# Performance work log

Measured on AMD Instinct MI355X. Metric: run time of the kernel, lower is better.

## Reference

```python
import jax, jax.numpy as jnp
import numpy as np

B, T, D = 32, 512, 240
HF, PF = 1024, 512
HB, PB = 1024, 512
BWD_BLOCK = 32
CLIP = 1.0


def setup_inputs() -> dict:
    key = jax.random.key(0)
    ks = jax.random.split(key, 8)
    u = lambda k, shape: jax.random.uniform(k, shape, jnp.float32, -0.05, 0.05)
    return {
        "data": jax.random.normal(ks[0], (B, T, D), jnp.float32),
        "mask": jnp.ones((B, T), jnp.float32),
        "weight_x_fwd": u(ks[1], (4 * HF, D)),
        "weight_r_fwd": u(ks[2], (4 * HF, PF)),
        "weight_bias_fwd": jnp.zeros((1, 4 * HF), jnp.float32),
        "weight_p_fwd": u(ks[3], (PF, HF)),
        "weight_x_bwd": u(ks[4], (4 * HB, D)),
        "weight_r_bwd": u(ks[5], (4 * HB, PB)),
        "weight_bias_bwd": jnp.zeros((1, 4 * HB), jnp.float32),
        "weight_p_bwd": u(ks[6], (PB, HB)),
    }


def _lstmp_scan(xg, wr, wp, mask, clip, hidden):
    """LSTM-with-projection scan.
    xg:   [T, N, 4H] precomputed input-side gate pre-activations (incl. bias)
    wr:   [4H, P] recurrent weights acting on projected state
    wp:   [P, H] projection weights
    mask: [T, N, 1] float mask (state held where mask==0)
    """
    N = xg.shape[1]
    P = wp.shape[0]
    c0 = jnp.zeros((N, hidden), xg.dtype)
    r0 = jnp.zeros((N, P), xg.dtype)

    def step(carry, inp):
        c, r = carry
        gx, m = inp
        gates = gx + r @ wr.T                      # [N, 4H]
        i, f, g, o = jnp.split(gates, 4, axis=-1)
        i = jax.nn.sigmoid(i)
        f = jax.nn.sigmoid(f)
        g = jnp.tanh(g)
        o = jax.nn.sigmoid(o)
        c_new = jnp.clip(f * c + i * g, -clip, clip)  # cell clipping
        r_new = (o * jnp.tanh(c_new)) @ wp.T          # project H -> P
        c = m * c_new + (1.0 - m) * c
        r = m * r_new + (1.0 - m) * r
        return (c, r), r

    _, rs = jax.lax.scan(step, (c0, r0), (xg, mask))
    return rs  # [T, N, P]


def reference(data, mask, weight_x_fwd, weight_r_fwd, weight_bias_fwd, weight_p_fwd,
              weight_x_bwd, weight_r_bwd, weight_bias_bwd, weight_p_bwd):
    Bx, Tx, _ = data.shape
    m = mask[..., None]  # [B, T, 1]

    # ---- forward direction: full left-to-right scan ----
    xg_f = jnp.einsum('btd,gd->tbg', data, weight_x_fwd) + weight_bias_fwd[0]
    m_f = jnp.swapaxes(m, 0, 1)  # [T, B, 1]
    out_f = _lstmp_scan(xg_f, weight_r_fwd, weight_p_fwd, m_f, CLIP, HF)
    out_f = jnp.swapaxes(out_f, 0, 1)  # [B, T, PF]

    # ---- backward direction: right-to-left within blocks of BWD_BLOCK ----
    L = BWD_BLOCK
    nb = Tx // L
    xg_b = jnp.einsum('btd,gd->btg', data, weight_x_bwd) + weight_bias_bwd[0]
    # split into blocks and reverse time within each block; blocks become batch
    xg_b = xg_b.reshape(Bx, nb, L, 4 * HB)[:, :, ::-1]
    xg_b = xg_b.transpose(2, 0, 1, 3).reshape(L, Bx * nb, 4 * HB)
    m_b = m.reshape(Bx, nb, L, 1)[:, :, ::-1].transpose(2, 0, 1, 3).reshape(L, Bx * nb, 1)
    out_b = _lstmp_scan(xg_b, weight_r_bwd, weight_p_bwd, m_b, CLIP, HB)
    out_b = out_b.reshape(L, Bx, nb, PB).transpose(1, 2, 0, 3)[:, :, ::-1]
    out_b = out_b.reshape(Bx, Tx, PB)

    return jnp.concatenate([out_f, out_b], axis=-1)  # [B, T, PF+PB]
```

## Files before the change

kernel.cpp:

```cpp
#include <hip/hip_runtime.h>
#include <hip/hip_bf16.h>
#include <math.h>


typedef __bf16 bf16_t;
typedef __bf16 bf16x8 __attribute__((ext_vector_type(8)));
typedef float f32x4 __attribute__((ext_vector_type(4)));
typedef unsigned int uint32;
typedef unsigned long long u64;

#define DEV __device__ __forceinline__

DEV bf16x8 ldg8(const bf16_t* p) { return *reinterpret_cast<const bf16x8*>(p); }
DEV bf16x8 ld_llc8(const bf16_t* p) {
  union { bf16x8 v; u64 q[2]; } u;
  u64* pp = (u64*)p;
  u.q[0] = __hip_atomic_load(pp, __ATOMIC_RELAXED, __HIP_MEMORY_SCOPE_AGENT);
  u.q[1] = __hip_atomic_load(pp + 1, __ATOMIC_RELAXED, __HIP_MEMORY_SCOPE_AGENT);
  return u.v;
}
DEV void st_llc_u32(uint32* p, uint32 v) {
  __hip_atomic_store(p, v, __ATOMIC_RELAXED, __HIP_MEMORY_SCOPE_AGENT);
}
DEV f32x4 mfma16(bf16x8 a, bf16x8 b, f32x4 c) {
  return __builtin_amdgcn_mfma_f32_16x16x32_bf16(a, b, c, 0, 0, 0);
}
DEV float sigmoidf_(float x) { return 1.0f / (1.0f + __expf(-x)); }
DEV unsigned short bfbits(float x) {
  union { __bf16 b; unsigned short s; } u; u.b = (bf16_t)x; return u.s;
}

struct Params {
  const float* data;
  const float* mask;
  const float* wx_f; const float* wr_f; const float* bias_f; const float* wp_f;
  const float* wx_b; const float* wr_b; const float* bias_b; const float* wp_b;
  float* out;
  bf16_t* data_bf;
  bf16_t* Wf;
  bf16_t* Wb;
  bf16_t* wrf;
  bf16_t* wpT;
  bf16_t* wpf;
  bf16_t* wpb;
  float* bias_f_p;
  float* bias_b_p;
  bf16_t* h_hist;
  bf16_t* h_buf;
  bf16_t* r_buf;
  f32x4*  chb;
  int* fcnt;
  int* bcA;
  int* bcC;
};

DEV void poll_ge(int* p, int tgt) {
  while (__hip_atomic_load(p, __ATOMIC_RELAXED, __HIP_MEMORY_SCOPE_AGENT) < tgt)
    __builtin_amdgcn_s_sleep(1);
}
DEV void wait_slots(int* base, int nslots, int tgt, int tid) {
  if (tid < nslots) poll_ge(base + tid * 32, tgt);
  __syncthreads();
  asm volatile("" ::: "memory");
}
DEV void drain_sync() {
  asm volatile("s_waitcnt vmcnt(0)" ::: "memory");
  __syncthreads();
}
DEV void pub_add(int* slot) {
  __hip_atomic_fetch_add(slot, 1, __ATOMIC_RELAXED, __HIP_MEMORY_SCOPE_AGENT);
}

__global__ void k_data(Params P) {
  int idx = blockIdx.x * 256 + threadIdx.x;
  int k = idx & 255; int row = idx >> 8;
  float v = (k < 240) ? P.data[(size_t)row * 240 + k] : 0.0f;
  P.data_bf[idx] = (bf16_t)v;
}

__global__ void k_prep_w(Params P) {
  int idx = blockIdx.x * 256 + threadIdx.x;
  int n = 4096 * 512;
  if (idx < n) { P.wrf[idx] = (bf16_t)P.wr_f[idx]; return; }
  idx -= n; n = 1024 * 512;
  if (idx < n) { int h = idx >> 9, p = idx & 511;
                 P.wpT[idx] = (bf16_t)P.wp_f[(size_t)p * 1024 + h]; return; }
  idx -= n; n = 512 * 1024;
  if (idx < n) { P.wpf[idx] = (bf16_t)P.wp_f[idx]; return; }
  idx -= n; n = 512 * 1024;
  if (idx < n) { P.wpb[idx] = (bf16_t)P.wp_b[idx]; return; }
}

__global__ void k_packf(Params P) {
  int pr = blockIdx.x, k = threadIdx.x;
  int jj = pr >> 5, lr = pr & 31, grp = lr >> 3, uu = lr & 7;
  int grow = grp * 1024 + jj * 8 + uu;
  float v = (k < 240) ? P.wx_f[(size_t)grow * 240 + k] : 0.0f;
  P.Wf[(size_t)pr * 1280 + 1024 + k] = (bf16_t)v;
  if (k == 0) P.bias_f_p[pr] = P.bias_f[grow];
}

__global__ void k_packb(Params P) {
  int pr = blockIdx.x; int k = blockIdx.y * 256 + threadIdx.x;
  int ut = pr >> 8, rem = pr & 255, grp = rem >> 6, uu = rem & 63;
  int grow = grp * 1024 + ut * 64 + uu;
  float v;
  if (k < 512) v = P.wr_b[(size_t)grow * 512 + k];
  else { int kx = k - 512; v = (kx < 240) ? P.wx_b[(size_t)grow * 240 + kx] : 0.0f; }
  P.Wb[(size_t)pr * 768 + k] = (bf16_t)v;
  if (k == 0) P.bias_b_p[pr] = P.bias_b[grow];
}

__global__ void wc_gemm(Params P) {
  int tid = threadIdx.x, lane = tid & 63, wave = tid >> 6;
  int lane15 = lane & 15, laneh = lane >> 4;
  int mt = blockIdx.x >> 4, nt = blockIdx.x & 15;
  f32x4 acc[4] = {};
  for (int kc = 0; kc < 16; ++kc) {
    int kl = kc * 32 + laneh * 8;
    bf16x8 bv = ldg8(P.wpT + (size_t)(nt * 64 + wave * 16 + lane15) * 512 + kl);
#pragma unroll
    for (int mh = 0; mh < 4; ++mh) {
      bf16x8 av = ldg8(P.wrf + (size_t)(mt * 64 + mh * 16 + lane15) * 512 + kl);
      acc[mh] = mfma16(av, bv, acc[mh]);
    }
  }
#pragma unroll
  for (int mh = 0; mh < 4; ++mh)
#pragma unroll
    for (int q = 0; q < 4; ++q) {
      int m = mt * 64 + mh * 16 + laneh * 4 + q;
      int grp = m >> 10, unit = m & 1023, jj = unit >> 3, u8 = unit & 7;
      int pr = jj * 32 + grp * 8 + u8;
      int ncol = nt * 64 + wave * 16 + lane15;
      P.Wf[(size_t)pr * 1280 + ncol] = (bf16_t)acc[mh][q];
    }
}

__global__ void __launch_bounds__(256, 1) scan_kernel(Params P) {
  __shared__ union SM {
    float red[4][2][2][16][16];
    float gates[4][64][64];
  } sm;
  const int tid = threadIdx.x;
  const int lane = tid & 63, wave = tid >> 6;
  const int lane15 = lane & 15, laneh = lane >> 4;

  if (blockIdx.x < 128) {
    const int j = blockIdx.x;
    const bf16_t* Wfp = P.Wf + (size_t)(j * 32) * 1280;
    bf16x8 wh[2][8], wx[2][2];
#pragma unroll
    for (int nh = 0; nh < 2; ++nh) {
#pragma unroll
      for (int kc = 0; kc < 8; ++kc)
        wh[nh][kc] = ldg8(Wfp + (size_t)(nh * 16 + lane15) * 1280 +
                          wave * 256 + kc * 32 + laneh * 8);
#pragma unroll
      for (int kc = 0; kc < 2; ++kc)
        wx[nh][kc] = ldg8(Wfp + (size_t)(nh * 16 + lane15) * 1280 +
                          1024 + wave * 64 + kc * 32 + laneh * 8);
    }
    const int cb = tid >> 2, up = tid & 3;
    float biasr[2][4];
    if (tid < 128) {
#pragma unroll
      for (int e = 0; e < 2; ++e)
#pragma unroll
        for (int g = 0; g < 4; ++g)
          biasr[e][g] = P.bias_f_p[j * 32 + g * 8 + 2 * up + e];
    }
    float c_st[2] = {0.f, 0.f}, h_st[2] = {0.f, 0.f};

    for (int t = 0; t < 512; ++t) {
      f32x4 acc[2][2] = {};
      {
        bf16x8 ax[2][2];
#pragma unroll
        for (int kc = 0; kc < 2; ++kc) {
          int kx = wave * 64 + kc * 32 + laneh * 8;
          ax[0][kc] = ldg8(P.data_bf + ((size_t)(lane15 * 512 + t)) * 256 + kx);
          ax[1][kc] = ldg8(P.data_bf + ((size_t)((16 + lane15) * 512 + t)) * 256 + kx);
        }
#pragma unroll
        for (int kc = 0; kc < 2; ++kc)
#pragma unroll
          for (int m = 0; m < 2; ++m) {
            acc[m][0] = mfma16(ax[m][kc], wx[0][kc], acc[m][0]);
            acc[m][1] = mfma16(ax[m][kc], wx[1][kc], acc[m][1]);
          }
      }
      if (t > 0) {
        wait_slots(P.fcnt + (size_t)(t - 1) * 512, 16, 8, tid);
        const bf16_t* hrow = P.h_hist + (size_t)(t - 1) * 32768;
        bf16x8 ah[2][8];
#pragma unroll
        for (int kc = 0; kc < 8; ++kc) {
          int kl = wave * 256 + kc * 32 + laneh * 8;
          ah[0][kc] = ldg8(hrow + (size_t)lane15 * 1024 + kl);
          ah[1][kc] = ldg8(hrow + (size_t)(16 + lane15) * 1024 + kl);
        }
#pragma unroll
        for (int kc = 0; kc < 8; ++kc)
#pragma unroll
          for (int m = 0; m < 2; ++m) {
            acc[m][0] = mfma16(ah[m][kc], wh[0][kc], acc[m][0]);
            acc[m][1] = mfma16(ah[m][kc], wh[1][kc], acc[m][1]);
          }
      } else {
        __syncthreads();
      }
#pragma unroll
      for (int m = 0; m < 2; ++m)
#pragma unroll
        for (int nh = 0; nh < 2; ++nh)
#pragma unroll
          for (int q = 0; q < 4; ++q)
            sm.red[wave][m][nh][laneh * 4 + q][lane15] = acc[m][nh][q];
      __syncthreads();

      if (tid < 128) {
        float mk = P.mask[cb * 512 + t];
        uint32 pk = 0;
#pragma unroll
        for (int e = 0; e < 2; ++e) {
          float g4[4];
#pragma unroll
          for (int g = 0; g < 4; ++g) {
            int lr = g * 8 + 2 * up + e;
            float v = biasr[e][g];
#pragma unroll
            for (int w2 = 0; w2 < 4; ++w2)
              v += sm.red[w2][cb >> 4][lr >> 4][cb & 15][lr & 15];
            g4[g] = v;
          }
          float iv = sigmoidf_(g4[0]);
          float fv = sigmoidf_(g4[1]);
          float gv = tanhf(g4[2]);
          float ov = sigmoidf_(g4[3]);
          float cnew = fminf(1.0f, fmaxf(-1.0f, fv * c_st[e] + iv * gv));
          float hnew = ov * tanhf(cnew);
          c_st[e] = mk * cnew + (1.0f - mk) * c_st[e];
          h_st[e] = mk * hnew + (1.0f - mk) * h_st[e];
          pk |= ((uint32)bfbits(h_st[e])) << (16 * e);
        }
        st_llc_u32((uint32*)(P.h_hist + (size_t)t * 32768 + cb * 1024 + j * 8 + 2 * up), pk);
      }
      drain_sync();
      if (tid == 0) pub_add(&P.fcnt[((size_t)t * 16 + (j & 15)) * 32]);
    }
  } else {
    const int bx = blockIdx.x - 128;
    const int btA = bx >> 4, utA = bx & 15;
    const int btC = bx >> 3, ptC = bx & 7;
    const int un = tid & 31, nr = tid >> 5;
    float biasB[2][4];
#pragma unroll
    for (int e = 0; e < 2; ++e)
#pragma unroll
      for (int g = 0; g < 4; ++g)
        biasB[e][g] = P.bias_b_p[utA * 256 + g * 64 + 2 * un + e];

    for (int s = 0; s < 32; ++s) {
      if (s > 0) {
        if (tid < 2) poll_ge(P.bcC + (size_t)(s - 1) * 512 + (btA * 2 + tid) * 32, 8);
        __syncthreads();
        asm volatile("" ::: "memory");
      } else {
        __syncthreads();
      }
      f32x4 acc[4][4] = {};
      const bf16_t* WbBase = P.Wb + (size_t)(utA * 256 + wave * 64) * 768;
      for (int kc = 0; kc < 24; ++kc) {
        int kb = kc * 32;
        if (kb < 512 && s == 0) continue;
        int kl = kb + laneh * 8;
        bf16x8 av[4];
        if (kb < 512) {
#pragma unroll
          for (int mh = 0; mh < 4; ++mh)
            av[mh] = ld_llc8(P.r_buf + (size_t)(btA * 64 + mh * 16 + lane15) * 512 + kl);
        } else {
          int kx = kl - 512;
#pragma unroll
          for (int mh = 0; mh < 4; ++mh) {
            int n = btA * 64 + mh * 16 + lane15;
            int t2 = (n & 15) * 32 + 31 - s;
            av[mh] = ldg8(P.data_bf + ((size_t)((n >> 4) * 512 + t2)) * 256 + kx);
          }
        }
#pragma unroll
        for (int nf = 0; nf < 4; ++nf) {
          bf16x8 bv = ldg8(WbBase + (size_t)(nf * 16 + lane15) * 768 + kl);
#pragma unroll
          for (int mh = 0; mh < 4; ++mh)
            acc[mh][nf] = mfma16(av[mh], bv, acc[mh][nf]);
        }
      }
#pragma unroll
      for (int mh = 0; mh < 4; ++mh)
#pragma unroll
        for (int nf = 0; nf < 4; ++nf)
#pragma unroll
          for (int q = 0; q < 4; ++q)
            sm.gates[wave][mh * 16 + laneh * 4 + q][nf * 16 + lane15] = acc[mh][nf][q];
      __syncthreads();

      for (int ii = 0; ii < 8; ++ii) {
        int n = ii * 8 + nr;
        int ng = btA * 64 + n;
        int b = ng >> 4;
        int t2 = (ng & 15) * 32 + 31 - s;
        float mk = P.mask[b * 512 + t2];
        size_t cix = (size_t)ng * 512 + utA * 32 + un;
        f32x4 chv;
        if (s == 0) { chv[0] = 0.f; chv[1] = 0.f; chv[2] = 0.f; chv[3] = 0.f; }
        else chv = P.chb[cix];
        uint32 pk = 0;
#pragma unroll
        for (int e = 0; e < 2; ++e) {
          float gi = sm.gates[0][n][2 * un + e] + biasB[e][0];
          float gf = sm.gates[1][n][2 * un + e] + biasB[e][1];
          float gg = sm.gates[2][n][2 * un + e] + biasB[e][2];
          float go = sm.gates[3][n][2 * un + e] + biasB[e][3];
          float iv = sigmoidf_(gi), fv = sigmoidf_(gf);
          float gv = tanhf(gg), ov = sigmoidf_(go);
          float cold = chv[2 * e], hold = chv[2 * e + 1];
          float cnew = fminf(1.0f, fmaxf(-1.0f, fv * cold + iv * gv));
          float hnew = ov * tanhf(cnew);
          float cm = mk * cnew + (1.0f - mk) * cold;
          float hm = mk * hnew + (1.0f - mk) * hold;
          chv[2 * e] = cm; chv[2 * e + 1] = hm;
          pk |= ((uint32)bfbits(hm)) << (16 * e);
        }
        P.chb[cix] = chv;
        st_llc_u32((uint32*)(P.h_buf + (size_t)ng * 1024 + utA * 64 + 2 * un), pk);
      }
      drain_sync();
      if (tid == 0) pub_add(&P.bcA[((size_t)s * 8 + btA) * 32]);

      if (tid == 0) poll_ge(P.bcA + (size_t)s * 256 + (btC >> 1) * 32, 16);
      __syncthreads();
      asm volatile("" ::: "memory");
      f32x4 acc2[2] = {};
      for (int kc = 0; kc < 32; ++kc) {
        int kl = kc * 32 + laneh * 8;
        bf16x8 bv = ldg8(P.wpb + (size_t)(ptC * 64 + wave * 16 + lane15) * 1024 + kl);
        bf16x8 a0 = ld_llc8(P.h_buf + (size_t)(btC * 32 + lane15) * 1024 + kl);
        bf16x8 a1 = ld_llc8(P.h_buf + (size_t)(btC * 32 + 16 + lane15) * 1024 + kl);
        acc2[0] = mfma16(a0, bv, acc2[0]);
        acc2[1] = mfma16(a1, bv, acc2[1]);
      }
#pragma unroll
      for (int mh = 0; mh < 2; ++mh)
#pragma unroll
        for (int q = 0; q < 4; ++q) {
          int nl = mh * 16 + laneh * 4 + q;
          int ng = btC * 32 + nl;
          int b = ng >> 4;
          int t2 = (ng & 15) * 32 + 31 - s;
          int p = ptC * 64 + wave * 16 + lane15;
          float v = acc2[mh][q];
          P.out[((size_t)b * 512 + t2) * 1024 + 512 + p] = v;
          float v2 = __shfl_xor(v, 1);
          if (!(lane & 1)) {
            uint32 pk = ((uint32)bfbits(v2) << 16) | bfbits(v);
            st_llc_u32((uint32*)(P.r_buf + (size_t)ng * 512 + p), pk);
          }
        }
      drain_sync();
      if (tid == 0) pub_add(&P.bcC[((size_t)s * 16 + btC) * 32]);
    }
  }
}

__global__ void fwd_proj(Params P) {
  int tid = threadIdx.x, lane = tid & 63, wave = tid >> 6;
  int lane15 = lane & 15, laneh = lane >> 4;
  int mt = blockIdx.x >> 3, nt = blockIdx.x & 7;
  f32x4 acc[4] = {};
  for (int kc = 0; kc < 32; ++kc) {
    int kl = kc * 32 + laneh * 8;
    bf16x8 bv = ldg8(P.wpf + (size_t)(nt * 64 + wave * 16 + lane15) * 1024 + kl);
#pragma unroll
    for (int mh = 0; mh < 4; ++mh) {
      bf16x8 av = ldg8(P.h_hist + (size_t)(mt * 64 + mh * 16 + lane15) * 1024 + kl);
      acc[mh] = mfma16(av, bv, acc[mh]);
    }
  }
#pragma unroll
  for (int mh = 0; mh < 4; ++mh)
#pragma unroll
    for (int q = 0; q < 4; ++q) {
      int m = mt * 64 + mh * 16 + laneh * 4 + q;
      int t = m >> 5, nb = m & 31;
      int p = nt * 64 + wave * 16 + lane15;
      P.out[((size_t)nb * 512 + t) * 1024 + p] = acc[mh][q];
    }
}

extern "C" void kernel_launch(void* const* d_in, const int* in_sizes, int n_in,
                              void* d_out, int out_size, void* d_ws, size_t ws_size,
                              hipStream_t stream) {
  (void)in_sizes; (void)n_in; (void)out_size; (void)ws_size;
  Params P;
  P.data   = (const float*)d_in[0];
  P.mask   = (const float*)d_in[1];
  P.wx_f   = (const float*)d_in[2];
  P.wr_f   = (const float*)d_in[3];
  P.bias_f = (const float*)d_in[4];
  P.wp_f   = (const float*)d_in[5];
  P.wx_b   = (const float*)d_in[6];
  P.wr_b   = (const float*)d_in[7];
  P.bias_b = (const float*)d_in[8];
  P.wp_b   = (const float*)d_in[9];
  P.out    = (float*)d_out;

  char* ws = (char*)d_ws;
  size_t o = 0;
  auto take = [&](size_t bytes) -> char* {
    char* p = ws + o; o += (bytes + 255) & ~(size_t)255; return p;
  };
  P.data_bf  = (bf16_t*)take(32ull * 512 * 256 * 2);
  P.Wf       = (bf16_t*)take(4096ull * 1280 * 2);
  P.Wb       = (bf16_t*)take(4096ull * 768 * 2);
  P.wrf      = (bf16_t*)take(4096ull * 512 * 2);
  P.wpT      = (bf16_t*)take(1024ull * 512 * 2);
  P.wpf      = (bf16_t*)take(512ull * 1024 * 2);
  P.wpb      = (bf16_t*)take(512ull * 1024 * 2);
  P.bias_f_p = (float*)take(4096 * 4);
  P.bias_b_p = (float*)take(4096 * 4);
  P.h_hist   = (bf16_t*)take(512ull * 32 * 1024 * 2);
  P.h_buf    = (bf16_t*)take(512ull * 1024 * 2);
  P.r_buf    = (bf16_t*)take(512ull * 512 * 2);
  P.chb      = (f32x4*)take(512ull * 512 * 16);
  size_t fcnt_i = 512ull * 16 * 32, bcA_i = 32ull * 8 * 32, bcC_i = 32ull * 16 * 32;
  char* cnts = take((fcnt_i + bcA_i + bcC_i) * 4);
  P.fcnt = (int*)cnts;
  P.bcA  = (int*)(cnts + fcnt_i * 4);
  P.bcC  = (int*)(cnts + (fcnt_i + bcA_i) * 4);

  hipMemsetAsync(cnts, 0, (fcnt_i + bcA_i + bcC_i) * 4, stream);
  k_data<<<16384, 256, 0, stream>>>(P);
  k_prep_w<<<14336, 256, 0, stream>>>(P);
  k_packf<<<4096, 256, 0, stream>>>(P);
  k_packb<<<dim3(4096, 3), 256, 0, stream>>>(P);
  wc_gemm<<<1024, 256, 0, stream>>>(P);
  scan_kernel<<<256, 256, 0, stream>>>(P);
  fwd_proj<<<2048, 256, 0, stream>>>(P);
}
```

Measured before the change: 2.544 ms.

## Replace forward-scan counter barriers with sentinel-polled h_hist and wider blocks

After: 4.077 ms. 1.6x slower.

```diff
diff --git a/kernel.cpp b/kernel.cpp
--- a/kernel.cpp
+++ b/kernel.cpp
@@ -12,11 +12,16 @@
 #define DEV __device__ __forceinline__
 
 DEV bf16x8 ldg8(const bf16_t* p) { return *reinterpret_cast<const bf16x8*>(p); }
+DEV u64 ld_a64(const u64* p) {
+  return __hip_atomic_load(p, __ATOMIC_RELAXED, __HIP_MEMORY_SCOPE_AGENT);
+}
+DEV void st_a64(u64* p, u64 v) {
+  __hip_atomic_store(p, v, __ATOMIC_RELAXED, __HIP_MEMORY_SCOPE_AGENT);
+}
 DEV bf16x8 ld_llc8(const bf16_t* p) {
   union { bf16x8 v; u64 q[2]; } u;
   u64* pp = (u64*)p;
-  u.q[0] = __hip_atomic_load(pp, __ATOMIC_RELAXED, __HIP_MEMORY_SCOPE_AGENT);
-  u.q[1] = __hip_atomic_load(pp + 1, __ATOMIC_RELAXED, __HIP_MEMORY_SCOPE_AGENT);
+  u.q[0] = ld_a64(pp); u.q[1] = ld_a64(pp + 1);
   return u.v;
 }
 DEV void st_llc_u32(uint32* p, uint32 v) {
@@ -26,6 +31,10 @@
   return __builtin_amdgcn_mfma_f32_16x16x32_bf16(a, b, c, 0, 0, 0);
 }
 DEV float sigmoidf_(float x) { return 1.0f / (1.0f + __expf(-x)); }
+DEV float tanhf_(float x) {
+  float e = __expf(2.0f * x);
+  return (e - 1.0f) / (e + 1.0f);
+}
 DEV unsigned short bfbits(float x) {
   union { __bf16 b; unsigned short s; } u; u.b = (bf16_t)x; return u.s;
 }
@@ -49,7 +58,6 @@
   bf16_t* h_buf;
   bf16_t* r_buf;
   f32x4*  chb;
-  int* fcnt;
   int* bcA;
   int* bcC;
 };
@@ -57,11 +65,6 @@
 DEV void poll_ge(int* p, int tgt) {
   while (__hip_atomic_load(p, __ATOMIC_RELAXED, __HIP_MEMORY_SCOPE_AGENT) < tgt)
     __builtin_amdgcn_s_sleep(1);
-}
-DEV void wait_slots(int* base, int nslots, int tgt, int tid) {
-  if (tid < nslots) poll_ge(base + tid * 32, tgt);
-  __syncthreads();
-  asm volatile("" ::: "memory");
 }
 DEV void drain_sync() {
   asm volatile("s_waitcnt vmcnt(0)" ::: "memory");
@@ -93,8 +96,8 @@
 
 __global__ void k_packf(Params P) {
   int pr = blockIdx.x, k = threadIdx.x;
-  int jj = pr >> 5, lr = pr & 31, grp = lr >> 3, uu = lr & 7;
-  int grow = grp * 1024 + jj * 8 + uu;
+  int jj = pr >> 6, lr = pr & 63, grp = lr >> 4, uu = lr & 15;
+  int grow = grp * 1024 + jj * 16 + uu;
   float v = (k < 240) ? P.wx_f[(size_t)grow * 240 + k] : 0.0f;
   P.Wf[(size_t)pr * 1280 + 1024 + k] = (bf16_t)v;
   if (k == 0) P.bias_f_p[pr] = P.bias_f[grow];
@@ -130,8 +133,8 @@
 #pragma unroll
     for (int q = 0; q < 4; ++q) {
       int m = mt * 64 + mh * 16 + laneh * 4 + q;
-      int grp = m >> 10, unit = m & 1023, jj = unit >> 3, u8 = unit & 7;
-      int pr = jj * 32 + grp * 8 + u8;
+      int grp = m >> 10, unit = m & 1023, jj = unit >> 4, u16 = unit & 15;
+      int pr = jj * 64 + grp * 16 + u16;
       int ncol = nt * 64 + wave * 16 + lane15;
       P.Wf[(size_t)pr * 1280 + ncol] = (bf16_t)acc[mh][q];
     }
@@ -139,19 +142,19 @@
 
 __global__ void __launch_bounds__(256, 1) scan_kernel(Params P) {
   __shared__ union SM {
-    float red[4][2][2][16][16];
+    float red[4][2][4][16][17];
     float gates[4][64][64];
   } sm;
   const int tid = threadIdx.x;
   const int lane = tid & 63, wave = tid >> 6;
   const int lane15 = lane & 15, laneh = lane >> 4;
 
-  if (blockIdx.x < 128) {
+  if (blockIdx.x < 64) {
     const int j = blockIdx.x;
-    const bf16_t* Wfp = P.Wf + (size_t)(j * 32) * 1280;
-    bf16x8 wh[2][8], wx[2][2];
-#pragma unroll
-    for (int nh = 0; nh < 2; ++nh) {
+    const bf16_t* Wfp = P.Wf + (size_t)(j * 64) * 1280;
+    bf16x8 wh[4][8], wx[4][2];
+#pragma unroll
+    for (int nh = 0; nh < 4; ++nh) {
 #pragma unroll
       for (int kc = 0; kc < 8; ++kc)
         wh[nh][kc] = ldg8(Wfp + (size_t)(nh * 16 + lane15) * 1280 +
@@ -161,19 +164,30 @@
         wx[nh][kc] = ldg8(Wfp + (size_t)(nh * 16 + lane15) * 1280 +
                           1024 + wave * 64 + kc * 32 + laneh * 8);
     }
-    const int cb = tid >> 2, up = tid & 3;
+    const int cb = tid >> 3, up = tid & 7;
     float biasr[2][4];
-    if (tid < 128) {
-#pragma unroll
-      for (int e = 0; e < 2; ++e)
-#pragma unroll
-        for (int g = 0; g < 4; ++g)
-          biasr[e][g] = P.bias_f_p[j * 32 + g * 8 + 2 * up + e];
-    }
+#pragma unroll
+    for (int e = 0; e < 2; ++e)
+#pragma unroll
+      for (int g = 0; g < 4; ++g)
+        biasr[e][g] = P.bias_f_p[j * 64 + g * 16 + 2 * up + e];
     float c_st[2] = {0.f, 0.f}, h_st[2] = {0.f, 0.f};
 
     for (int t = 0; t < 512; ++t) {
-      f32x4 acc[2][2] = {};
+      const bf16_t* hrow = P.h_hist + (size_t)(t - 1) * 32768;
+      u64 q[2][8][2];
+      if (t > 0) {
+#pragma unroll
+        for (int m = 0; m < 2; ++m)
+#pragma unroll
+          for (int kc = 0; kc < 8; ++kc) {
+            u64* p = (u64*)(hrow + (size_t)(m * 16 + lane15) * 1024 +
+                            wave * 256 + kc * 32 + laneh * 8);
+            q[m][kc][0] = ld_a64(p);
+            q[m][kc][1] = ld_a64(p + 1);
+          }
+      }
+      f32x4 acc[2][4] = {};
       {
         bf16x8 ax[2][2];
 #pragma unroll
@@ -185,72 +199,94 @@
 #pragma unroll
         for (int kc = 0; kc < 2; ++kc)
 #pragma unroll
-          for (int m = 0; m < 2; ++m) {
-            acc[m][0] = mfma16(ax[m][kc], wx[0][kc], acc[m][0]);
-            acc[m][1] = mfma16(ax[m][kc], wx[1][kc], acc[m][1]);
+          for (int m = 0; m < 2; ++m)
+#pragma unroll
+            for (int nh = 0; nh < 4; ++nh)
+              acc[m][nh] = mfma16(ax[m][kc], wx[nh][kc], acc[m][nh]);
+      }
+      if (t > 0) {
+        bf16x8 ah[2][8];
+        uint32 rem = 0;
+#pragma unroll
+        for (int m = 0; m < 2; ++m)
+#pragma unroll
+          for (int kc = 0; kc < 8; ++kc) {
+            int gi = m * 8 + kc;
+            u64 q0 = q[m][kc][0], q1 = q[m][kc][1];
+            if (q0 != ~0ull && q1 != ~0ull) {
+              union { u64 qq[2]; bf16x8 v; } u; u.qq[0] = q0; u.qq[1] = q1;
+              ah[m][kc] = u.v;
+            } else rem |= 1u << gi;
           }
-      }
-      if (t > 0) {
-        wait_slots(P.fcnt + (size_t)(t - 1) * 512, 16, 8, tid);
-        const bf16_t* hrow = P.h_hist + (size_t)(t - 1) * 32768;
-        bf16x8 ah[2][8];
-#pragma unroll
-        for (int kc = 0; kc < 8; ++kc) {
-          int kl = wave * 256 + kc * 32 + laneh * 8;
-          ah[0][kc] = ldg8(hrow + (size_t)lane15 * 1024 + kl);
-          ah[1][kc] = ldg8(hrow + (size_t)(16 + lane15) * 1024 + kl);
+        while (rem) {
+          __builtin_amdgcn_s_sleep(1);
+#pragma unroll
+          for (int m = 0; m < 2; ++m)
+#pragma unroll
+            for (int kc = 0; kc < 8; ++kc) {
+              int gi = m * 8 + kc;
+              if (rem & (1u << gi)) {
+                u64* p = (u64*)(hrow + (size_t)(m * 16 + lane15) * 1024 +
+                                wave * 256 + kc * 32 + laneh * 8);
+                u64 q0 = ld_a64(p), q1 = ld_a64(p + 1);
+                if (q0 != ~0ull && q1 != ~0ull) {
+                  union { u64 qq[2]; bf16x8 v; } u; u.qq[0] = q0; u.qq[1] = q1;
+                  ah[m][kc] = u.v;
+                  rem &= ~(1u << gi);
+                }
+              }
+            }
         }
 #pragma unroll
         for (int kc = 0; kc < 8; ++kc)
 #pragma unroll
-          for (int m = 0; m < 2; ++m) {
-            acc[m][0] = mfma16(ah[m][kc], wh[0][kc], acc[m][0]);
-            acc[m][1] = mfma16(ah[m][kc], wh[1][kc], acc[m][1]);
-          }
-      } else {
-        __syncthreads();
+          for (int m = 0; m < 2; ++m)
+#pragma unroll
+            for (int nh = 0; nh < 4; ++nh)
+              acc[m][nh] = mfma16(ah[m][kc], wh[nh][kc], acc[m][nh]);
       }
 #pragma unroll
       for (int m = 0; m < 2; ++m)
 #pragma unroll
-        for (int nh = 0; nh < 2; ++nh)
-#pragma unroll
-          for (int q = 0; q < 4; ++q)
-            sm.red[wave][m][nh][laneh * 4 + q][lane15] = acc[m][nh][q];
+        for (int nh = 0; nh < 4; ++nh)
+#pragma unroll
+          for (int qd = 0; qd < 4; ++qd)
+            sm.red[wave][m][nh][laneh * 4 + qd][lane15] = acc[m][nh][qd];
       __syncthreads();
 
-      if (tid < 128) {
-        float mk = P.mask[cb * 512 + t];
-        uint32 pk = 0;
-#pragma unroll
-        for (int e = 0; e < 2; ++e) {
-          float g4[4];
-#pragma unroll
-          for (int g = 0; g < 4; ++g) {
-            int lr = g * 8 + 2 * up + e;
-            float v = biasr[e][g];
-#pragma unroll
-            for (int w2 = 0; w2 < 4; ++w2)
-              v += sm.red[w2][cb >> 4][lr >> 4][cb & 15][lr & 15];
-            g4[g] = v;
-          }
-          float iv = sigmoidf_(g4[0]);
-          float fv = sigmoidf_(g4[1]);
-          float gv = tanhf(g4[2]);
-          float ov = sigmoidf_(g4[3]);
-          float cnew = fminf(1.0f, fmaxf(-1.0f, fv * c_st[e] + iv * gv));
-          float hnew = ov * tanhf(cnew);
-          c_st[e] = mk * cnew + (1.0f - mk) * c_st[e];
-          h_st[e] = mk * hnew + (1.0f - mk) * h_st[e];
-          pk |= ((uint32)bfbits(h_st[e])) << (16 * e);
-        }
-        st_llc_u32((uint32*)(P.h_hist + (size_t)t * 32768 + cb * 1024 + j * 8 + 2 * up), pk);
-      }
-      drain_sync();
-      if (tid == 0) pub_add(&P.fcnt[((size_t)t * 16 + (j & 15)) * 32]);
+      float mk = P.mask[cb * 512 + t];
+      uint32 pk = 0;
+#pragma unroll
+      for (int e = 0; e < 2; ++e) {
+        int u = 2 * up + e;
+        float g4[4];
+#pragma unroll
+        for (int g = 0; g < 4; ++g) {
+          float v = biasr[e][g];
+#pragma unroll
+          for (int wv = 0; wv < 4; ++wv)
+            v += sm.red[wv][cb >> 4][g][cb & 15][u];
+          g4[g] = v;
+        }
+        float iv = sigmoidf_(g4[0]);
+        float fv = sigmoidf_(g4[1]);
+        float gv = tanhf_(g4[2]);
+        float ov = sigmoidf_(g4[3]);
+        float cnew = fminf(1.0f, fmaxf(-1.0f, fv * c_st[e] + iv * gv));
+        float hnew = ov * tanhf_(cnew);
+        c_st[e] = mk * cnew + (1.0f - mk) * c_st[e];
+        h_st[e] = mk * hnew + (1.0f - mk) * h_st[e];
+        pk |= ((uint32)bfbits(h_st[e])) << (16 * e);
+      }
+      __syncthreads();
+      uint32 po = __shfl_xor((int)pk, 1);
+      if (!(up & 1)) {
+        u64 qq = (u64)pk | ((u64)po << 32);
+        st_a64((u64*)(P.h_hist + (size_t)t * 32768 + cb * 1024 + j * 16 + 2 * up), qq);
+      }
     }
   } else {
-    const int bx = blockIdx.x - 128;
+    const int bx = blockIdx.x - 64;
     const int btA = bx >> 4, utA = bx & 15;
     const int btC = bx >> 3, ptC = bx & 7;
     const int un = tid & 31, nr = tid >> 5;
@@ -324,10 +360,10 @@
           float gg = sm.gates[2][n][2 * un + e] + biasB[e][2];
           float go = sm.gates[3][n][2 * un + e] + biasB[e][3];
           float iv = sigmoidf_(gi), fv = sigmoidf_(gf);
-          float gv = tanhf(gg), ov = sigmoidf_(go);
+          float gv = tanhf_(gg), ov = sigmoidf_(go);
           float cold = chv[2 * e], hold = chv[2 * e + 1];
           float cnew = fminf(1.0f, fmaxf(-1.0f, fv * cold + iv * gv));
-          float hnew = ov * tanhf(cnew);
+          float hnew = ov * tanhf_(cnew);
           float cm = mk * cnew + (1.0f - mk) * cold;
           float hm = mk * hnew + (1.0f - mk) * hold;
           chv[2 * e] = cm; chv[2 * e + 1] = hm;
@@ -434,18 +470,18 @@
   P.h_buf    = (bf16_t*)take(512ull * 1024 * 2);
   P.r_buf    = (bf16_t*)take(512ull * 512 * 2);
   P.chb      = (f32x4*)take(512ull * 512 * 16);
-  size_t fcnt_i = 512ull * 16 * 32, bcA_i = 32ull * 8 * 32, bcC_i = 32ull * 16 * 32;
-  char* cnts = take((fcnt_i + bcA_i + bcC_i) * 4);
-  P.fcnt = (int*)cnts;
-  P.bcA  = (int*)(cnts + fcnt_i * 4);
-  P.bcC  = (int*)(cnts + (fcnt_i + bcA_i) * 4);
-
-  hipMemsetAsync(cnts, 0, (fcnt_i + bcA_i + bcC_i) * 4, stream);
+  size_t bcA_i = 32ull * 8 * 32, bcC_i = 32ull * 16 * 32;
+  char* cnts = take((bcA_i + bcC_i) * 4);
+  P.bcA  = (int*)cnts;
+  P.bcC  = (int*)(cnts + bcA_i * 4);
+
+  hipMemsetAsync(cnts, 0, (bcA_i + bcC_i) * 4, stream);
+  hipMemsetAsync(P.h_hist, 0xFF, 512ull * 32 * 1024 * 2, stream);
   k_data<<<16384, 256, 0, stream>>>(P);
   k_prep_w<<<14336, 256, 0, stream>>>(P);
   k_packf<<<4096, 256, 0, stream>>>(P);
   k_packb<<<dim3(4096, 3), 256, 0, stream>>>(P);
   wc_gemm<<<1024, 256, 0, stream>>>(P);
-  scan_kernel<<<256, 256, 0, stream>>>(P);
+  scan_kernel<<<192, 256, 0, stream>>>(P);
   fwd_proj<<<2048, 256, 0, stream>>>(P);
 }
```

## Replace atomic step counters with per-block flag stores and use fast tanh

Applied to the files above, without the earlier changes.

Result: no change. 2.510 ms (-1.3%).

```diff
diff --git a/kernel.cpp b/kernel.cpp
--- a/kernel.cpp
+++ b/kernel.cpp
@@ -26,6 +26,10 @@
   return __builtin_amdgcn_mfma_f32_16x16x32_bf16(a, b, c, 0, 0, 0);
 }
 DEV float sigmoidf_(float x) { return 1.0f / (1.0f + __expf(-x)); }
+DEV float tanhf_(float x) {
+  float e = __expf(2.0f * x);
+  return (e - 1.0f) / (e + 1.0f);
+}
 DEV unsigned short bfbits(float x) {
   union { __bf16 b; unsigned short s; } u; u.b = (bf16_t)x; return u.s;
 }
@@ -58,17 +62,12 @@
   while (__hip_atomic_load(p, __ATOMIC_RELAXED, __HIP_MEMORY_SCOPE_AGENT) < tgt)
     __builtin_amdgcn_s_sleep(1);
 }
-DEV void wait_slots(int* base, int nslots, int tgt, int tid) {
-  if (tid < nslots) poll_ge(base + tid * 32, tgt);
-  __syncthreads();
-  asm volatile("" ::: "memory");
+DEV void st_slot(int* p, int v) {
+  __hip_atomic_store(p, v, __ATOMIC_RELAXED, __HIP_MEMORY_SCOPE_AGENT);
 }
 DEV void drain_sync() {
   asm volatile("s_waitcnt vmcnt(0)" ::: "memory");
   __syncthreads();
-}
-DEV void pub_add(int* slot) {
-  __hip_atomic_fetch_add(slot, 1, __ATOMIC_RELAXED, __HIP_MEMORY_SCOPE_AGENT);
 }
 
 __global__ void k_data(Params P) {
@@ -139,7 +138,7 @@
 
 __global__ void __launch_bounds__(256, 1) scan_kernel(Params P) {
   __shared__ union SM {
-    float red[4][2][2][16][16];
+    float red[4][2][2][16][17];
     float gates[4][64][64];
   } sm;
   const int tid = threadIdx.x;
@@ -191,7 +190,9 @@
           }
       }
       if (t > 0) {
-        wait_slots(P.fcnt + (size_t)(t - 1) * 512, 16, 8, tid);
+        if (tid < 128) poll_ge(P.fcnt + tid * 16, t);
+        __syncthreads();
+        asm volatile("" ::: "memory");
         const bf16_t* hrow = P.h_hist + (size_t)(t - 1) * 32768;
         bf16x8 ah[2][8];
 #pragma unroll
@@ -236,10 +237,10 @@
           }
           float iv = sigmoidf_(g4[0]);
           float fv = sigmoidf_(g4[1]);
-          float gv = tanhf(g4[2]);
+          float gv = tanhf_(g4[2]);
           float ov = sigmoidf_(g4[3]);
           float cnew = fminf(1.0f, fmaxf(-1.0f, fv * c_st[e] + iv * gv));
-          float hnew = ov * tanhf(cnew);
+          float hnew = ov * tanhf_(cnew);
           c_st[e] = mk * cnew + (1.0f - mk) * c_st[e];
           h_st[e] = mk * hnew + (1.0f - mk) * h_st[e];
           pk |= ((uint32)bfbits(h_st[e])) << (16 * e);
@@ -247,7 +248,7 @@
         st_llc_u32((uint32*)(P.h_hist + (size_t)t * 32768 + cb * 1024 + j * 8 + 2 * up), pk);
       }
       drain_sync();
-      if (tid == 0) pub_add(&P.fcnt[((size_t)t * 16 + (j & 15)) * 32]);
+      if (tid == 0) st_slot(&P.fcnt[j * 16], t + 1);
     }
   } else {
     const int bx = blockIdx.x - 128;
@@ -263,7 +264,10 @@
 
     for (int s = 0; s < 32; ++s) {
       if (s > 0) {
-        if (tid < 2) poll_ge(P.bcC + (size_t)(s - 1) * 512 + (btA * 2 + tid) * 32, 8);
+        if (tid < 16) {
+          int bxp = (btA * 2 + (tid >> 3)) * 8 + (tid & 7);
+          poll_ge(P.bcC + bxp * 16, s);
+        }
         __syncthreads();
         asm volatile("" ::: "memory");
       } else {
@@ -324,10 +328,10 @@
           float gg = sm.gates[2][n][2 * un + e] + biasB[e][2];
           float go = sm.gates[3][n][2 * un + e] + biasB[e][3];
           float iv = sigmoidf_(gi), fv = sigmoidf_(gf);
-          float gv = tanhf(gg), ov = sigmoidf_(go);
+          float gv = tanhf_(gg), ov = sigmoidf_(go);
           float cold = chv[2 * e], hold = chv[2 * e + 1];
           float cnew = fminf(1.0f, fmaxf(-1.0f, fv * cold + iv * gv));
-          float hnew = ov * tanhf(cnew);
+          float hnew = ov * tanhf_(cnew);
           float cm = mk * cnew + (1.0f - mk) * cold;
           float hm = mk * hnew + (1.0f - mk) * hold;
           chv[2 * e] = cm; chv[2 * e + 1] = hm;
@@ -337,9 +341,9 @@
         st_llc_u32((uint32*)(P.h_buf + (size_t)ng * 1024 + utA * 64 + 2 * un), pk);
       }
       drain_sync();
-      if (tid == 0) pub_add(&P.bcA[((size_t)s * 8 + btA) * 32]);
-
-      if (tid == 0) poll_ge(P.bcA + (size_t)s * 256 + (btC >> 1) * 32, 16);
+      if (tid == 0) st_slot(&P.bcA[bx * 16], s + 1);
+
+      if (tid < 16) poll_ge(P.bcA + ((btC >> 1) * 16 + tid) * 16, s + 1);
       __syncthreads();
       asm volatile("" ::: "memory");
       f32x4 acc2[2] = {};
@@ -369,7 +373,7 @@
           }
         }
       drain_sync();
-      if (tid == 0) pub_add(&P.bcC[((size_t)s * 16 + btC) * 32]);
+      if (tid == 0) st_slot(&P.bcC[bx * 16], s + 1);
     }
   }
 }
@@ -434,13 +438,13 @@
   P.h_buf    = (bf16_t*)take(512ull * 1024 * 2);
   P.r_buf    = (bf16_t*)take(512ull * 512 * 2);
   P.chb      = (f32x4*)take(512ull * 512 * 16);
-  size_t fcnt_i = 512ull * 16 * 32, bcA_i = 32ull * 8 * 32, bcC_i = 32ull * 16 * 32;
-  char* cnts = take((fcnt_i + bcA_i + bcC_i) * 4);
+  size_t slot_i = 128ull * 16;
+  char* cnts = take(3 * slot_i * 4);
   P.fcnt = (int*)cnts;
-  P.bcA  = (int*)(cnts + fcnt_i * 4);
-  P.bcC  = (int*)(cnts + (fcnt_i + bcA_i) * 4);
-
-  hipMemsetAsync(cnts, 0, (fcnt_i + bcA_i + bcC_i) * 4, stream);
+  P.bcA  = (int*)(cnts + slot_i * 4);
+  P.bcC  = (int*)(cnts + 2 * slot_i * 4);
+
+  hipMemsetAsync(cnts, 0, 3 * slot_i * 4, stream);
   k_data<<<16384, 256, 0, stream>>>(P);
   k_prep_w<<<14336, 256, 0, stream>>>(P);
   k_packf<<<4096, 256, 0, stream>>>(P);
```
